# Optimization experiments

Measured on AMD Instinct MI355X. Metric: run time of the kernel, lower is better.

Reference implementation:

```python
import jax, jax.numpy as jnp
import numpy as np

N, B, PG, L, HC, EC, H, NC, KNN = 256, 4, 64, 32, 128, 64, 4, 14, 8
D = HC // H
CUTOFF = 10.0
LOG2 = 0.6931471805599453

_counts = np.array([14, 5, 11, 8, 8, 6, 9, 9, 4, 10, 8, 8, 9, 8, 11, 7, 6, 7, 14, 12, 7])
RES_ATOM_MASK = (np.arange(14)[None, :] < _counts[:, None]).astype(np.float32)  # [21,14]


def _ln(x, g, b):
    mu = jnp.mean(x, -1, keepdims=True)
    var = jnp.mean((x - mu) ** 2, -1, keepdims=True)
    return (x - mu) / jnp.sqrt(var + 1e-5) * g + b


def _ssp(x):
    return jax.nn.softplus(x) - LOG2


def _safe_norm(x):
    return jnp.sqrt(jnp.maximum(jnp.sum(x * x, -1), 1e-12))


def _seg_softmax(x, idx, n):
    m = jax.ops.segment_max(x, idx, num_segments=n)
    e = jnp.exp(x - m[idx])
    s = jax.ops.segment_sum(e, idx, num_segments=n)
    return e / s[idx]


def _smear(d):
    offs = jnp.linspace(0.0, CUTOFF, EC)
    coeff = -0.5 / (offs[1] - offs[0]) ** 2
    return jnp.exp(coeff * (d[..., None] - offs) ** 2)


def _core(res_H, res_X, ligand_pos, ligand_feat, ligand_mask,
          ln_g, ln_b, ln1_g, ln1_b,
          WQ, WK, WV, WKl, WVl, WO, WOl, WOl1,
          Ti_w1, Ti_b1, Ti_w2, Ti_b2,
          sD_w1, sD_b1, sD_w2, sD_b2,
          sD1_w1, sD1_b1, sD1_w2, sD1_b2,
          res_S, batch, residue_mask, row1, col1):
    n = res_H.shape[0]
    bsz = ligand_feat.shape[0]
    lc = ligand_feat.shape[1]
    amask = jnp.asarray(RES_ATOM_MASK)[res_S]  # [n,14]

    # kNN graph on C-alpha (atom 1), per-graph, flow target_to_source, + self loops
    ctr = res_X[:, 1]
    d2 = jnp.sum((ctr[:, None] - ctr[None]) ** 2, -1)
    bad = (batch[:, None] != batch[None]) | jnp.eye(n, dtype=bool)
    _, nbr = jax.lax.top_k(-jnp.where(bad, jnp.inf, d2), KNN)
    row = jnp.concatenate([jnp.repeat(jnp.arange(n), KNN), jnp.arange(n)])
    col = jnp.concatenate([nbr.reshape(-1), jnp.arange(n)])

    Rij = _safe_norm(res_X[row][:, :, None] - res_X[col][:, None])  # [E,14,14]
    drep = _smear(Rij)  # [E,14,14,EC]

    res_Hn = _ln(res_H, ln_g, ln_b)
    Q = (res_Hn @ WQ.T).reshape(n, NC, H, D)
    Kt = (res_Hn @ WK.T).reshape(n, NC, H, D)
    V = (res_Hn @ WV.T).reshape(n, NC, H, D)

    logits = jnp.einsum('ephd,eqhd->ehpq', Q[row], Kt[col]) / np.sqrt(D)
    sig = jax.nn.relu(drep @ sD_w1.T + sD_b1) @ sD_w2.T + sD_b2  # [E,14,14,H]
    logits = logits + sig.transpose(0, 3, 1, 2)

    am_e = amask[row][:, :, None] * amask[col][:, None]  # [E,14,14]
    r = jnp.einsum('ep,ehpq,eq->eh', amask[row], logits, amask[col])
    r = r / jnp.sum(am_e, (-1, -2))[:, None]
    beta = _seg_softmax(r, row, n)  # [E,H]

    att = jax.nn.softmax(logits, -1) * am_e[:, None]
    att = att / (jnp.sum(jnp.abs(att), -1, keepdims=True) + 1e-7)
    aV = jnp.einsum('ehpq,eqhd->ehpd', att, V[col])
    updH = jax.ops.segment_sum(beta[:, :, None, None] * aV, row, num_segments=n)
    updH = updH.transpose(0, 2, 1, 3).reshape(n, NC, HC)
    res_H2 = (res_Hn + _ssp(updH) @ WO.T) * amask[..., None]

    Xij = res_X[row][:, :, None] - res_X[col][:, None]  # [E,14,14,3]
    Xij = Xij / (_safe_norm(Xij)[..., None] + 1e-5)
    Qf = Q.reshape(n, NC, HC)
    Kf = Kt.reshape(n, NC, HC)
    # T_i on concat([Q_p, K_q, dist]) computed as split matmuls (no big concat)
    hmid = (Qf[row] @ Ti_w1[:, :HC].T)[:, :, None, :] \
        + (Kf[col] @ Ti_w1[:, HC:2 * HC].T)[:, None, :, :] \
        + drep @ Ti_w1[:, 2 * HC:].T + Ti_b1  # [E,14,14,HC]
    f = (jax.nn.relu(hmid) @ Ti_w2.T + Ti_b2)[..., 0]  # [E,14,14]
    f = f * jnp.mean(att, 1)
    dX = jax.ops.segment_sum(jnp.mean(beta, -1)[:, None, None]
                             * jnp.sum(f[..., None] * Xij, -2), row, num_segments=n)
    res_X2 = jnp.where(residue_mask[:, None, None],
                       res_X + jnp.clip(dX, -3.0, 3.0), res_X)

    # residue <-> ligand cross attention over (editable residue, graph) edges
    lf = _ln(ligand_feat, ln1_g, ln1_b)
    Kl = (lf @ WKl.T).reshape(bsz, lc, H, D)
    Vl = (lf @ WVl.T).reshape(bsz, lc, H, D)
    Rij1 = _safe_norm(res_X2[row1][:, :, None] - ligand_pos[col1][:, None])
    drep1 = _smear(Rij1)  # [E1,14,L,EC]
    lg = jnp.einsum('ephd,eqhd->ehpq', Q[row1], Kl[col1]) / np.sqrt(D)
    sig1 = jax.nn.relu(drep1 @ sD1_w1.T + sD1_b1) @ sD1_w2.T + sD1_b2
    lg = lg + sig1.transpose(0, 3, 1, 2)

    am1 = amask[row1][:, :, None] * ligand_mask[col1][:, None]  # [E1,14,L]
    r1 = jnp.einsum('ep,ehpq,eq->eh', amask[row1], lg, ligand_mask[col1])
    r1 = r1 / jnp.sum(am1, (-1, -2))[:, None]
    beta1 = _seg_softmax(r1, col1, bsz)

    ar = jax.nn.softmax(lg, -1) * am1[:, None]
    ar = ar / (jnp.sum(jnp.abs(ar), -1, keepdims=True) + 1e-7)
    al = jax.nn.softmax(lg, -2) * am1[:, None]
    # faithful to source: lig branch divided by L1 norm of already-normalized ar
    al = al / (jnp.sum(jnp.abs(ar), -1, keepdims=True) + 1e-7)
    aVr = jnp.einsum('ehpq,eqhd->ehpd', ar, Vl[col1])  # [E1,H,14,D]
    e1 = row1.shape[0]
    res_H3 = res_H2.at[row1].add(
        _ssp(aVr.transpose(0, 2, 1, 3).reshape(e1, NC, HC)) @ WOl.T)
    res_H3 = res_H3 * amask[..., None]
    aVlg = jnp.einsum('ehpq,ephd->ehqd', al, V[row1])  # [E1,H,L,D]
    updL = jax.ops.segment_sum(beta1[:, :, None, None] * aVlg, col1, num_segments=bsz)
    lf2 = lf + _ssp(updL.transpose(0, 2, 1, 3).reshape(bsz, lc, HC)) @ WOl1.T
    return res_H3, res_X2, lf2


def setup_inputs() -> dict:
    key = jax.random.key(0)
    ks = jax.random.split(key, 40)
    rn = lambda i, shape, s=1.0: jax.random.normal(ks[i], shape, jnp.float32) * s
    w = lambda i, shape: jax.random.normal(ks[i], shape, jnp.float32) * 0.05
    res_H = rn(0, (N, NC, HC))
    res_X = rn(1, (N, NC, 3), 4.0)
    res_S = jax.random.randint(ks[2], (N,), 0, 21)
    batch = jnp.repeat(jnp.arange(B), PG)
    residue_mask = (jnp.arange(N) % PG) < 16
    row1 = jnp.asarray(np.nonzero(np.asarray(residue_mask))[0])
    col1 = row1 // PG
    ligand_pos = rn(3, (B, L, 3), 4.0)
    ligand_feat = rn(4, (B, L, HC))
    ligand_mask = jnp.tile((jnp.arange(L) < 24).astype(jnp.float32)[None], (B, 1))
    return dict(
        res_H=res_H, res_X=res_X, ligand_pos=ligand_pos, ligand_feat=ligand_feat,
        ligand_mask=ligand_mask,
        ln_g=jnp.ones((HC,)), ln_b=jnp.zeros((HC,)),
        ln1_g=jnp.ones((HC,)), ln1_b=jnp.zeros((HC,)),
        WQ=w(5, (HC, HC)), WK=w(6, (HC, HC)), WV=w(7, (HC, HC)),
        WKl=w(8, (HC, HC)), WVl=w(9, (HC, HC)),
        WO=w(10, (HC, HC)), WOl=w(11, (HC, HC)), WOl1=w(12, (HC, HC)),
        Ti_w1=w(13, (HC, 2 * HC + EC)), Ti_b1=jnp.zeros((HC,)),
        Ti_w2=w(14, (1, HC)), Ti_b2=jnp.zeros((1,)),
        sD_w1=w(15, (HC, EC)), sD_b1=jnp.zeros((HC,)),
        sD_w2=w(16, (H, HC)), sD_b2=jnp.zeros((H,)),
        sD1_w1=w(17, (HC, EC)), sD1_b1=jnp.zeros((HC,)),
        sD1_w2=w(18, (H, HC)), sD1_b2=jnp.zeros((H,)),
        res_S=res_S, batch=batch, residue_mask=residue_mask, row1=row1, col1=col1)


def reference(res_H, res_X, ligand_pos, ligand_feat, ligand_mask,
              ln_g, ln_b, ln1_g, ln1_b,
              WQ, WK, WV, WKl, WVl, WO, WOl, WOl1,
              Ti_w1, Ti_b1, Ti_w2, Ti_b2,
              sD_w1, sD_b1, sD_w2, sD_b2,
              sD1_w1, sD1_b1, sD1_w2, sD1_b2,
              res_S, batch, residue_mask, row1, col1):
    return _core(res_H, res_X, ligand_pos, ligand_feat, ligand_mask,
                 ln_g, ln_b, ln1_g, ln1_b,
                 WQ, WK, WV, WKl, WVl, WO, WOl, WOl1,
                 Ti_w1, Ti_b1, Ti_w2, Ti_b2,
                 sD_w1, sD_b1, sD_w2, sD_b2,
                 sD1_w1, sD1_b1, sD1_w2, sD1_b2,
                 res_S, batch, residue_mask, row1, col1)
```

## Files before the change

kernel.cpp:

```cpp
#include <hip/hip_runtime.h>
#include <hip/hip_bf16.h>
#include <math.h>

typedef __hip_bfloat16 bf16;

#define NRES 256
#define LC   32
#define HCH  128
#define ECH  64
#define NH   4
#define NCA  14
#define KNNK 8
#define DH   32
#define NKE  (NRES*KNNK)
#define NEDGE (NKE+NRES)
#define NE1  64
#define NROWS (NRES*NCA)

#define NT     3073
#define TSCALE 256.0f
#define DMAXT  12.0f

#define O_RESH   0
#define O_RESX   458752
#define O_LPOS   469504
#define O_LFEAT  469888
#define O_LMASK  486272
#define O_LNG    486400
#define O_LNB    486528
#define O_LN1G   486656
#define O_LN1B   486784
#define O_WQ     486912
#define O_WK     503296
#define O_WV     519680
#define O_WKL    536064
#define O_WVL    552448
#define O_WO     568832
#define O_WOL    585216
#define O_WOL1   601600
#define O_TIW1   617984
#define O_TIB1   658944
#define O_TIW2   659072
#define O_TIB2   659200
#define O_SDW1   659204
#define O_SDB1   667396
#define O_SDW2   667524
#define O_SDB2   668036
#define O_SD1W1  668040
#define O_SD1B1  676232
#define O_SD1W2  676360
#define O_SD1B2  676872
#define TOTCVT   676876
#define CVT_RSV  676880

#define OUTX_OFF 458752
#define OUTL_OFF 469504

#define NGEMM 291
#define FCV   476
#define FG0   (FCV+1)
#define FTR0  (FG0+NGEMM)
#define FTOT  (FTR0+640)

__constant__ int c_counts[21] = {14,5,11,8,8,6,9,9,4,10,8,8,9,8,11,7,6,7,14,12,7};

using bfrag = __attribute__((ext_vector_type(8))) short;
using f32x4 = __attribute__((ext_vector_type(4))) float;

__device__ __forceinline__ float b2f(bf16 x){ return __bfloat162float(x); }
__device__ __forceinline__ float sspf(float x){
  return fmaxf(x,0.f) + log1pf(expf(-fabsf(x))) - 0.6931471805599453f;
}
__device__ __forceinline__ float bflo(unsigned u){ return __uint_as_float(u<<16); }
__device__ __forceinline__ float bfhi(unsigned u){ return __uint_as_float(u & 0xffff0000u); }
__device__ __forceinline__ unsigned short f2bs(float v){ bf16 b=__float2bfloat16(v); return *(unsigned short*)&b; }
__device__ __forceinline__ unsigned pack2(float a, float b){
  return (unsigned)f2bs(a) | ((unsigned)f2bs(b)<<16);
}
__device__ __forceinline__ int ccount(int s){ return c_counts[s<0?0:(s>20?20:s)]; }
__device__ __forceinline__ void storeOut(void* out, int isbf, int idx, float v){
  if (isbf) ((bf16*)out)[idx] = __float2bfloat16(v);
  else      ((float*)out)[idx] = v;
}
__device__ __forceinline__ float rdv(const void* p, int isbf, int i){
  return isbf ? b2f(((const bf16*)p)[i]) : ((const float*)p)[i];
}

__global__ __launch_bounds__(256) void kfront(
    const void* s0,const void* s1,const void* s2,const void* s3,const void* s4,
    const void* s5,const void* s6,const void* s7,const void* s8,const void* s9,
    const void* s10,const void* s11,const void* s12,const void* s13,const void* s14,
    const void* s15,const void* s16,const void* s17,const void* s18,const void* s19,
    const void* s20,const void* s21,const void* s22,const void* s23,const void* s24,
    const void* s25,const void* s26,const void* s27,const void* s28,
    const int* __restrict__ row1,
    float* __restrict__ dst, int* __restrict__ flag,
    unsigned* __restrict__ ctab, float* __restrict__ sig1T,
    float* __restrict__ wt, int* __restrict__ inv_row)
{
  int bb = blockIdx.x, tid = threadIdx.x;
  __shared__ int sflag;
  if (tid < 64){
    unsigned w = ((const unsigned*)s0)[tid];
    unsigned lo = w & 0xFFFFu;
    int ee = (lo >> 7) & 0xFF;
    int good = (lo == 0u) || (ee >= 121 && ee <= 133);
    unsigned long long m = __ballot(good);
    if (tid == 0){
      sflag = (__popcll(m) >= 40) ? 1 : 0;
      if (bb == 0) flag[0] = sflag;
    }
  }
  __syncthreads();
  int isbf = sflag;

  if (bb < FCV){
    int g0 = (bb*256 + tid)*4;
    if (g0 >= O_WQ) return;
    const void* src; int l;
    if      (g0 < O_RESX ) { src=s0; l=g0; }
    else if (g0 < O_LPOS ) { src=s1; l=g0-O_RESX; }
    else if (g0 < O_LFEAT) { src=s2; l=g0-O_LPOS; }
    else if (g0 < O_LMASK) { src=s3; l=g0-O_LFEAT; }
    else if (g0 < O_LNG  ) { src=s4; l=g0-O_LMASK; }
    else if (g0 < O_LNB  ) { src=s5; l=g0-O_LNG; }
    else if (g0 < O_LN1G ) { src=s6; l=g0-O_LNB; }
    else if (g0 < O_LN1B ) { src=s7; l=g0-O_LN1G; }
    else                   { src=s8; l=g0-O_LN1B; }
    float4 o4;
    if (isbf){
      uint2 u = *(const uint2*)((const unsigned short*)src + l);
      o4.x = bflo(u.x); o4.y = bfhi(u.x); o4.z = bflo(u.y); o4.w = bfhi(u.y);
    } else {
      o4 = *(const float4*)((const float*)src + l);
    }
    *(float4*)(dst + g0) = o4;
    return;
  }

  if (bb == FCV){
    if (tid < 132){
      int g = O_TIW2 + tid;
      float v = (g < O_TIB2) ? rdv(s19, isbf, g - O_TIW2) : rdv(s20, isbf, 0);
      dst[g] = v;
    }
    inv_row[tid] = -1;
    __syncthreads();
    if (tid < NE1) inv_row[row1[tid] & 255] = tid;
    return;
  }

  if (bb < FTR0){
    __shared__ float Wl[128*68];
    __shared__ float Et[32*68];
    __shared__ float H[32*132];
    __shared__ float W2[4*132];
    __shared__ float W2b[4];
    int gb = bb - FG0;
    int mt = gb % 97, m = gb / 97;
    int r0 = mt*32;
    int nr = (NT - r0 < 32) ? (NT - r0) : 32;

    for (int idx=tid; idx<8192; idx+=256){
      int o=idx>>6, k=idx&63;
      float v = (m==0) ? rdv(s17, isbf, o*320 + 256 + k)
              : (m==1) ? rdv(s21, isbf, idx)
                       : rdv(s25, isbf, idx);
      Wl[o*68+k] = v;
    }
    {
      const float step = 10.0f/63.0f;
      const float coef = -0.5f/(step*step);
      for (int idx=tid; idx<2048; idx+=256){
        int r=idx>>6, k=idx&63;
        float t = (float)(r0+r)*(1.0f/256.0f) - step*(float)k;
        Et[r*68+k] = expf(coef*t*t);
      }
    }
    if (m >= 1){
      const void* w2p = (m==1)? s23 : s27;
      const void* b2p = (m==1)? s24 : s28;
      for (int idx=tid; idx<512; idx+=256)
        W2[(idx>>7)*132 + (idx&127)] = rdv(w2p, isbf, idx);
      if (tid < 4) W2b[tid] = rdv(b2p, isbf, tid);
    }
    __syncthreads();

    int o = tid & 127, g = tid >> 7;
    const void* bp = (m==0)? s18 : (m==1)? s22 : s26;
    float bias = rdv(bp, isbf, o);
    float acc[16];
    #pragma unroll
    for (int i=0;i<16;i++) acc[i] = bias;
    const float* wrow = Wl + o*68;
    const float* ebase = Et + g*16*68;
    for (int kc=0; kc<16; kc++){
      float4 w4 = *(const float4*)(wrow + kc*4);
      #pragma unroll
      for (int i=0;i<16;i++){
        float4 e4 = *(const float4*)(ebase + i*68 + kc*4);
        acc[i] += e4.x*w4.x;
        acc[i] += e4.y*w4.y;
        acc[i] += e4.z*w4.z;
        acc[i] += e4.w*w4.w;
      }
    }

    if (m == 0){
      #pragma unroll
      for (int i=0;i<16;i++){
        int row = r0 + g*16 + i;
        float c = acc[i];
// ... 25 lines not shown
          float s1 = __shfl_down(s,1);
          float s2 = __shfl_down(s,2);
          float s3 = __shfl_down(s,3);
          if (hh == 0){
            ctab[(size_t)row*68 + 0] = pack2(s, s1);
            ctab[(size_t)row*68 + 1] = pack2(s2, s3);
          }
        } else {
          sig1T[row*4 + hh] = s;
        }
      }
    }
    return;
  }

  {
    int gid = (bb - FTR0)*256 + tid;
    int m = gid >> 14;
    int j = gid & 16383;
    int oo = j >> 7, c = j & 127;
    float v;
    switch(m){
      case 0: v = rdv(s9,  isbf, j); break;
      case 1: v = rdv(s10, isbf, j); break;
      case 2: v = rdv(s11, isbf, j); break;
      case 3: v = rdv(s14, isbf, j); break;
      case 4: v = rdv(s12, isbf, j); break;
      case 5: v = rdv(s13, isbf, j); break;
      case 6: v = rdv(s15, isbf, j); break;
      case 7: v = rdv(s16, isbf, j); break;
      case 8: v = rdv(s17, isbf, oo*320 + c); break;
      default:v = rdv(s17, isbf, oo*320 + 128 + c); break;
    }
    wt[m*16384 + c*128 + oo] = v;
  }
}

__global__ __launch_bounds__(256) void kProjAll(
    const float* __restrict__ cvt, const float* __restrict__ wt, const int* __restrict__ batch,
    float* __restrict__ resHn, bf16* __restrict__ Qw16, bf16* __restrict__ Kw16,
    bf16* __restrict__ Vw16, bf16* __restrict__ TQw16, bf16* __restrict__ TKw16,
    int* __restrict__ nbr, float* __restrict__ lf, bf16* __restrict__ Klw16, bf16* __restrict__ Vlw16)
{
  __shared__ float Xs[16*129];
  __shared__ float x2[2][HCH];
  __shared__ float sred2[2][2];
  int bb = blockIdx.x, tid = threadIdx.x;

  if (bb < 672){
    int m = bb / 224;
    int rt = (bb % 224) * 16;
    for (int i=tid; i<16*128; i+=256){
      int r=i>>7, c=i&127;
      Xs[r*129+c] = cvt[O_RESH + (rt+r)*HCH + c];
    }
    __syncthreads();
    {
      int wave = tid>>6, lane = tid&63;
      int r = wave*4 + (lane>>4);
      int cb = lane & 15;
      float s=0;
      #pragma unroll
      for (int j=0;j<8;j++) s += Xs[r*129 + cb + 16*j];
      #pragma unroll
      for (int off=1; off<16; off<<=1) s += __shfl_xor(s, off);
      float mu = s*(1.f/HCH);
      float q=0;
      #pragma unroll
      for (int j=0;j<8;j++){ float dv = Xs[r*129+cb+16*j]-mu; q += dv*dv; }
      #pragma unroll
      for (int off=1; off<16; off<<=1) q += __shfl_xor(q, off);
      float inv = rsqrtf(q*(1.f/HCH) + 1e-5f);
      #pragma unroll
      for (int j=0;j<8;j++){
        int c = cb + 16*j;
        float xh = (Xs[r*129+c]-mu)*inv*cvt[O_LNG+c] + cvt[O_LNB+c];
        Xs[r*129+c] = xh;
        if (m==0) resHn[(rt+r)*HCH+c] = xh;
      }
    }
    __syncthreads();
    int tc = (tid & 31) * 4;
    int tr = (tid >> 5) * 2;
    const float* W = wt + m*16384;
    float a00=0,a01=0,a02=0,a03=0, a10=0,a11=0,a12=0,a13=0;
    for (int c=0;c<HCH;c++){
      float4 w4 = *(const float4*)(W + c*128 + tc);
      float x0 = Xs[tr*129 + c];
      float x1 = Xs[(tr+1)*129 + c];
      a00 += x0*w4.x; a01 += x0*w4.y; a02 += x0*w4.z; a03 += x0*w4.w;
      a10 += x1*w4.x; a11 += x1*w4.y; a12 += x1*w4.z; a13 += x1*w4.w;
    }
    bf16* out = (m==0)? Qw16 : (m==1)? Kw16 : Vw16;
    {
      unsigned* o0 = (unsigned*)(out + (rt+tr  )*HCH + tc);
      unsigned* o1 = (unsigned*)(out + (rt+tr+1)*HCH + tc);
      o0[0]=pack2(a00,a01); o0[1]=pack2(a02,a03);
      o1[0]=pack2(a10,a11); o1[1]=pack2(a12,a13);
    }
    if (m == 2) return;
    __syncthreads();
    Xs[tr*129+tc]=a00; Xs[tr*129+tc+1]=a01; Xs[tr*129+tc+2]=a02; Xs[tr*129+tc+3]=a03;
    Xs[(tr+1)*129+tc]=a10; Xs[(tr+1)*129+tc+1]=a11; Xs[(tr+1)*129+tc+2]=a12; Xs[(tr+1)*129+tc+3]=a13;
    __syncthreads();
    const float* W2 = wt + (8+m)*16384;
    a00=0;a01=0;a02=0;a03=0; a10=0;a11=0;a12=0;a13=0;
    for (int c=0;c<HCH;c++){
      float4 w4 = *(const float4*)(W2 + c*128 + tc);
      float x0 = Xs[tr*129 + c];
      float x1 = Xs[(tr+1)*129 + c];
      a00 += x0*w4.x; a01 += x0*w4.y; a02 += x0*w4.z; a03 += x0*w4.w;
      a10 += x1*w4.x; a11 += x1*w4.y; a12 += x1*w4.z; a13 += x1*w4.w;
    }
    bf16* out2 = m ? TKw16 : TQw16;
    {
      unsigned* o0 = (unsigned*)(out2 + (rt+tr  )*HCH + tc);
      unsigned* o1 = (unsigned*)(out2 + (rt+tr+1)*HCH + tc);
      o0[0]=pack2(a00,a01); o0[1]=pack2(a02,a03);
      o1[0]=pack2(a10,a11); o1[1]=pack2(a12,a13);
    }
    return;
  }

  if (bb < 736){
    int wave = tid>>6, lane = tid&63;
    int n = (bb-672)*4 + wave;
    float cx = cvt[O_RESX+(n*NCA+1)*3+0];
    float cy = cvt[O_RESX+(n*NCA+1)*3+1];
    float cz = cvt[O_RESX+(n*NCA+1)*3+2];
    int bn = batch[n];
    float d2v[4]; int idv[4];
    #pragma unroll
    for (int t=0;t<4;t++){
      int j = lane + 64*t;
      float jx = cvt[O_RESX+(j*NCA+1)*3+0];
      float jy = cvt[O_RESX+(j*NCA+1)*3+1];
      float jz = cvt[O_RESX+(j*NCA+1)*3+2];
      float dx=cx-jx, dy=cy-jy, dz=cz-jz;
      float d2 = dx*dx+dy*dy+dz*dz;
      bool bad = (batch[j]!=bn) || (j==n);
      d2v[t] = bad ? INFINITY : d2;
      idv[t] = j;
    }
    for (int k=0;k<KNNK;k++){
      float dm = d2v[0]; int im = idv[0];
      #pragma unroll
      for (int t=1;t<4;t++)
        if (d2v[t]<dm || (d2v[t]==dm && idv[t]<im)){ dm=d2v[t]; im=idv[t]; }
      #pragma unroll
      for (int off=1; off<64; off<<=1){
        float dn = __shfl_xor(dm, off);
        int   in = __shfl_xor(im, off);
        if (dn<dm || (dn==dm && in<im)){ dm=dn; im=in; }
      }
      if (lane==0) nbr[n*KNNK+k] = im;
      #pragma unroll
      for (int t=0;t<4;t++) if (idv[t]==im) d2v[t] = INFINITY;
    }
    return;
  }

  int row = tid>>7, t = tid&127;
  int rb = (bb-736)*2 + row;
  float v = cvt[O_LFEAT + rb*HCH + t];
  float s=v;
  for (int off=1; off<64; off<<=1) s += __shfl_xor(s, off);
  if ((t&63)==0) sred2[row][t>>6]=s;
  __syncthreads();
  float mu=(sred2[row][0]+sred2[row][1])*(1.f/HCH);
  __syncthreads();
  float d=v-mu; s=d*d;
  for (int off=1; off<64; off<<=1) s += __shfl_xor(s, off);
  if ((t&63)==0) sred2[row][t>>6]=s;
  __syncthreads();
  float var=(sred2[row][0]+sred2[row][1])*(1.f/HCH);
  float xh = d*rsqrtf(var+1e-5f)*cvt[O_LN1G+t] + cvt[O_LN1B+t];
  x2[row][t]=xh; lf[rb*HCH+t]=xh;
  __syncthreads();
  const float* WKlt = wt + 4*16384;
  const float* WVlt = wt + 5*16384;
  float aK=0.f, aV=0.f;
  for (int c=0;c<HCH;c++){
    float xc=x2[row][c];
    aK += xc*WKlt[c*128+t];
    aV += xc*WVlt[c*128+t];
  }
  Klw16[rb*HCH+t]=__float2bfloat16(aK);
  Vlw16[rb*HCH+t]=__float2bfloat16(aV);
}

#define PR1(cbu, tau, kau, wl, wh) \
  fa += fmaxf(bflo(tau)+bflo(kau)+bflo(cbu),0.f)*(wl) + fmaxf(bfhi(tau)+bfhi(kau)+bfhi(cbu),0.f)*(wh);

__global__ __launch_bounds__(256) void k3_edge(
    const float* __restrict__ cvt, const int* __restrict__ res_S, const int* __restrict__ nbr,
    const bf16* __restrict__ Qw16, const bf16* __restrict__ Kw16,
    const bf16* __restrict__ TQw16, const bf16* __restrict__ TKw16,
    const bf16* __restrict__ Vw16, const unsigned* __restrict__ ctab,
    float* __restrict__ r_ws, bf16* __restrict__ aVe16, float* __restrict__ dXe)
{
  __shared__ __align__(16) unsigned char UB[8192];
  __shared__ unsigned Tqp[14*66], Tkp[14*66];
  __shared__ float LG[4*16*17];
// ... 195 lines not shown
    #pragma unroll
    for (int qq=0;qq<NCA;qq++){
      float diff = Xr[pp*3+jx]-Xc[qq*3+jx];
      a += FR[pp*14+qq]*diff;
    }
    dXe[(e*NCA+pp)*3+jx] = a;
  }
}

__global__ __launch_bounds__(256) void k4_agg(
    const float* __restrict__ cvt, const int* __restrict__ res_S, const int* __restrict__ inv_row,
    const float* __restrict__ r_ws, const bf16* __restrict__ aVe16, const float* __restrict__ dXe,
    const float* __restrict__ resHn, const float* __restrict__ wt, const int* __restrict__ flag,
    float* __restrict__ resH2, float* __restrict__ resX2, void* __restrict__ d_out)
{
  int n = blockIdx.x, tid = threadIdx.x;
  __shared__ float beta[9][NH];
  __shared__ float betam[9];
  __shared__ float Xs[NCA][HCH];
  if (tid < NH){
    int h = tid;
    float rv[9], m=-INFINITY;
    #pragma unroll
    for (int k=0;k<9;k++){
      int ek = (k<KNNK)? n*KNNK+k : NKE+n;
      rv[k] = r_ws[ek*NH+h];
      m = fmaxf(m, rv[k]);
    }
    float s=0;
    #pragma unroll
    for (int k=0;k<9;k++){ rv[k]=expf(rv[k]-m); s+=rv[k]; }
    #pragma unroll
    for (int k=0;k<9;k++) beta[k][h]=rv[k]/s;
  }
  __syncthreads();
  if (tid < 9) betam[tid] = 0.25f*(beta[tid][0]+beta[tid][1]+beta[tid][2]+beta[tid][3]);
  int col = tid & 127, ph = tid >> 7;
  int h = col>>5, dd = col&31;
  float bh[9];
  #pragma unroll
  for (int k=0;k<9;k++) bh[k]=beta[k][h];
  #pragma unroll
  for (int i=0;i<7;i++){
    int p = ph + 2*i;
    float u=0;
    #pragma unroll
    for (int k=0;k<9;k++){
      int ek = (k<KNNK)? n*KNNK+k : NKE+n;
      u += bh[k]*b2f(aVe16[ek*1792 + h*448 + p*32 + dd]);
    }
    Xs[p][col] = sspf(u);
  }
  __syncthreads();
  const float* WOt = wt + 3*16384;
  float acc[7];
  #pragma unroll
  for (int i=0;i<7;i++) acc[i]=0.f;
  for (int c=0;c<HCH;c++){
    float w = WOt[c*128+col];
    #pragma unroll
    for (int i=0;i<7;i++) acc[i] += Xs[ph+2*i][c]*w;
  }
  int cnt = ccount(res_S[n]);
  #pragma unroll
  for (int i=0;i<7;i++){
    int p = ph + 2*i;
    float am = (p<cnt)?1.f:0.f;
    float outv = (resHn[(n*NCA+p)*HCH+col] + acc[i])*am;
    resH2[(n*NCA+p)*HCH+col] = outv;
  }
  if (tid < NCA*3){
    int isbf = *flag;
    int p=tid/3, jx=tid%3;
    float s=0;
    #pragma unroll
    for (int k=0;k<9;k++){
      int ek=(k<KNNK)? n*KNNK+k : NKE+n;
      s += betam[k]*dXe[(ek*NCA+p)*3+jx];
    }
    float base = cvt[O_RESX+(n*NCA+p)*3+jx];
    float v = (inv_row[n]>=0) ? base + fminf(fmaxf(s,-3.f),3.f) : base;
    resX2[(n*NCA+p)*3+jx] = v;
    storeOut(d_out, isbf, OUTX_OFF + (n*NCA+p)*3+jx, v);
  }
}

// ... 37 lines not shown

  const float isq=0.17677669529663687f;
  for (int pair=tid; pair<448; pair+=256){
    int p=pair>>5, q=pair&31;
    float dx=Xr[p*3]-Lp[q*3], dy=Xr[p*3+1]-Lp[q*3+1], dz=Xr[p*3+2]-Lp[q*3+2];
    float d=sqrtf(fmaxf(dx*dx+dy*dy+dz*dz,1e-12f));
    int i0=(int)(fminf(d,DMAXT)*TSCALE+0.5f);
    float sg = sig1T[i0*4+h];
    float qk=0;
    #pragma unroll
    for (int dd=0;dd<DH;dd++) qk += Bq[p*33+dd]*Bk[q*33+dd];
    LG[p*33+q] = qk*isq + sg;
  }
  __syncthreads();

  if (tid < 14){
    int pp=tid; float ap=amr[pp];
    float s=0, m=-INFINITY;
    for (int qq=0;qq<LC;qq++){ float v=LG[pp*33+qq]; s+=v*lm[qq]; m=fmaxf(m,v); }
    rpart[pp]=s*ap;
    float sum=0;
    for (int qq=0;qq<LC;qq++) sum+=expf(LG[pp*33+qq]-m);
    float inv=1.f/sum, s2=0;
    for (int qq=0;qq<LC;qq++) s2+=expf(LG[pp*33+qq]-m)*inv*ap*lm[qq];
    s2r[pp]=s2/(s2+1e-7f);
  }
  if (tid==14){ float sr=0; for(int i=0;i<14;i++) sr+=amr[i]; cnts[0]=sr; }
  if (tid==15){ float sl=0; for(int i=0;i<32;i++) sl+=lm[i]; cnts[1]=sl; }
  __syncthreads();

  if (tid==0){ float s=0; for (int pp=0;pp<14;pp++) s+=rpart[pp]; r1_ws[e*NH+h]=s/(cnts[0]*cnts[1]); }
  if (tid < 32){
    int qq=tid;
    float m=-INFINITY;
    for (int pp=0;pp<14;pp++) m=fmaxf(m,LG[pp*33+qq]);
    float sum=0;
    for (int pp=0;pp<14;pp++) sum+=expf(LG[pp*33+qq]-m);
    float inv=1.f/sum, lq=lm[qq];
    for (int pp=0;pp<14;pp++){
      float a=expf(LG[pp*33+qq]-m)*inv*amr[pp]*lq;
      ALs[pp*33+qq]=a/(s2r[pp]+1e-7f);
    }
  }
  __syncthreads();

  if (tid < 14){
    int pp=tid; float ap=amr[pp];
    float m=-INFINITY;
    for (int qq=0;qq<LC;qq++) m=fmaxf(m,LG[pp*33+qq]);
    float row[LC]; float sum=0;
    for (int qq=0;qq<LC;qq++){ row[qq]=expf(LG[pp*33+qq]-m); sum+=row[qq]; }
    float inv=1.f/sum, s2=0;
    for (int qq=0;qq<LC;qq++){ row[qq]=row[qq]*inv*ap*lm[qq]; s2+=row[qq]; }
    float inv2=1.f/(s2+1e-7f);
    for (int qq=0;qq<LC;qq++) LG[pp*33+qq]=row[qq]*inv2;
  }
  __syncthreads();

  for (int j=tid;j<448;j+=256){
    int pp=j>>5, dd=j&31;
    float acc=0;
    #pragma unroll
    for (int qq=0;qq<LC;qq++) acc += LG[pp*33+qq]*Vls[qq*33+dd];
    aVr[e*1792 + h*448 + j]=acc;
  }
  for (int j=tid;j<1024;j+=256){
    int qq=j>>5, dd=j&31;
    float acc=0;
    #pragma unroll
    for (int pp=0;pp<14;pp++) acc += ALs[pp*33+qq]*Vrs[pp*33+dd];
    aVlg[e*4096 + h*1024 + j]=acc;
  }
}

__global__ __launch_bounds__(256) void k78_final(
    const int* __restrict__ inv_row, const int* __restrict__ res_S, const int* __restrict__ col1,
    const float* __restrict__ resH2, const float* __restrict__ aVr,
    const float* __restrict__ r1_ws, const float* __restrict__ aVlg, const float* __restrict__ lf,
    const float* __restrict__ wt, const int* __restrict__ flag, void* __restrict__ d_out)
{
  int bb = blockIdx.x, tid = threadIdx.x;
  if (bb < 256){
    int n = bb;
    int e = inv_row[n];
    __shared__ float G[NCA][HCH];
// ... 16 lines not shown
        for (int i=0;i<7;i++) acc[i]+=G[ph+2*i][c]*w;
      }
    }
    int cnt=ccount(res_S[n]);
    int isbf = *flag;
    #pragma unroll
    for (int i=0;i<7;i++){
      int p = ph + 2*i;
      float am=(p<cnt)?1.f:0.f;
      float v=(resH2[(n*NCA+p)*HCH+col]+acc[i])*am;
      storeOut(d_out, isbf, (n*NCA+p)*HCH+col, v);
    }
    return;
  }
  int rb = bb - 256;
  int b = rb>>5, q = rb&31;
  __shared__ float bw[NE1][NH];
  __shared__ float xs[HCH];
  if (tid<NH){
    int h=tid;
    float m=-INFINITY;
    for (int e=0;e<NE1;e++) if ((col1[e]&3)==b) m=fmaxf(m, r1_ws[e*NH+h]);
    float s=0;
    for (int e=0;e<NE1;e++) if ((col1[e]&3)==b) s+=expf(r1_ws[e*NH+h]-m);
    for (int e=0;e<NE1;e++) bw[e][h] = ((col1[e]&3)==b)? expf(r1_ws[e*NH+h]-m)/s : 0.f;
  }
  __syncthreads();
  if (tid < 128){
    int h=tid>>5, dd=tid&31;
    float u=0;
    for (int e=0;e<NE1;e++) u += bw[e][h]*aVlg[e*4096 + h*1024 + q*32 + dd];
    xs[tid]=sspf(u);
  }
  __syncthreads();
  if (tid < 128){
    const float* WOl1t = wt + 7*16384;
    float acc=0;
    for (int c=0;c<HCH;c++) acc += xs[c]*WOl1t[c*128+tid];
    float v = lf[rb*HCH+tid] + acc;
    storeOut(d_out, *flag, OUTL_OFF + rb*HCH+tid, v);
// ... 24 lines not shown
  bf16*  TKw16   = (bf16*)(wsf + o); o += NROWS*HCH/2;
  float* r_ws    = wsf + o; o += NEDGE*NH;
  bf16*  aVe16   = (bf16*)(wsf + o); o += (size_t)NEDGE*1792/2;
  float* dXe     = wsf + o; o += NEDGE*NCA*3;
  float* resH2   = wsf + o; o += NROWS*HCH;
  float* resX2   = wsf + o; o += NRES*NCA*3;
  float* lf      = wsf + o; o += 4*LC*HCH;
  bf16*  Klw16   = (bf16*)(wsf + o); o += 4*LC*HCH/2;
  bf16*  Vlw16   = (bf16*)(wsf + o); o += 4*LC*HCH/2;
  float* r1w     = wsf + o; o += NE1*NH;
  float* aVrw    = wsf + o; o += NE1*1792;
  float* aVlgw   = wsf + o; o += NE1*4096;
  unsigned* ctab = (unsigned*)(wsf + o); o += (size_t)NT*68;
  float* sig1T   = wsf + o; o += NT*4;

  kfront<<<FTOT, 256, 0, stream>>>(
      d_in[0],d_in[1],d_in[2],d_in[3],d_in[4],d_in[5],d_in[6],d_in[7],d_in[8],
      d_in[9],d_in[10],d_in[11],d_in[12],d_in[13],d_in[14],d_in[15],d_in[16],
      d_in[17],d_in[18],d_in[19],d_in[20],d_in[21],d_in[22],d_in[23],d_in[24],
      d_in[25],d_in[26],d_in[27],d_in[28],
      row1, cvt, flag, ctab, sig1T, wt, inv_row);
  kProjAll<<<800, 256, 0, stream>>>(cvt, wt, batch, resHn, Qw16, Kw16, Vw16, TQw16, TKw16,
                                    nbr, lf, Klw16, Vlw16);
  k3_edge<<<NEDGE, 256, 0, stream>>>(cvt, res_S, nbr, Qw16, Kw16, TQw16, TKw16, Vw16, ctab,
                                     r_ws, aVe16, dXe);
  k4_agg<<<NRES, 256, 0, stream>>>(cvt, res_S, inv_row, r_ws, aVe16, dXe, resHn, wt, flag,
                                   resH2, resX2, d_out);
  k6_lig<<<NE1*NH, 256, 0, stream>>>(cvt, res_S, row1, col1, resX2, Qw16, Klw16, Vw16, Vlw16, sig1T,
                                     r1w, aVrw, aVlgw);
  k78_final<<<384, 256, 0, stream>>>(inv_row, res_S, col1, resH2, aVrw, r1w, aVlgw, lf,
                                     wt, flag, d_out);
}
```

Measured before the change: 239.0 us.

## Merge projection kernel into front kernel and parallelize aggregation and softmax stages

Fuses the former kProjAll work (LayerNorm and Q/K/V/TQ/TK projections, kNN, ligand projections) into the front conversion kernel, reading raw inputs directly instead of the converted and transposed copies. This removes one kernel launch and the dependency on the conversion pass, at the cost of reading weights in their original layout from global memory. The edge-table GEMM also stops staging weights in shared memory. Separately, k4_agg is split over two blocks per residue, the k6_lig row softmax is spread across 224 threads with shuffle reductions instead of 14 serial threads, and the k78 ligand softmax weights are computed by all threads in parallel.

```diff
diff --git a/kernel.cpp b/kernel.cpp
--- a/kernel.cpp
+++ b/kernel.cpp
@@ -31,25 +31,8 @@
 #define O_LN1G   486656
 #define O_LN1B   486784
 #define O_WQ     486912
-#define O_WK     503296
-#define O_WV     519680
-#define O_WKL    536064
-#define O_WVL    552448
-#define O_WO     568832
-#define O_WOL    585216
-#define O_WOL1   601600
-#define O_TIW1   617984
-#define O_TIB1   658944
 #define O_TIW2   659072
 #define O_TIB2   659200
-#define O_SDW1   659204
-#define O_SDB1   667396
-#define O_SDW2   667524
-#define O_SDB2   668036
-#define O_SD1W1  668040
-#define O_SD1B1  676232
-#define O_SD1W2  676360
-#define O_SD1B2  676872
 #define TOTCVT   676876
 #define CVT_RSV  676880
 
@@ -60,7 +43,10 @@
 #define FCV   476
 #define FG0   (FCV+1)
 #define FTR0  (FG0+NGEMM)
-#define FTOT  (FTR0+640)
+#define FPJ0  (FTR0+640)
+#define FKN0  (FPJ0+672)
+#define FLG0  (FKN0+64)
+#define FBTOT (FLG0+64)
 
 __constant__ int c_counts[21] = {14,5,11,8,8,6,9,9,4,10,8,8,9,8,11,7,6,7,14,12,7};
 
@@ -85,21 +71,36 @@
 __device__ __forceinline__ float rdv(const void* p, int isbf, int i){
   return isbf ? b2f(((const bf16*)p)[i]) : ((const float*)p)[i];
 }
-
-__global__ __launch_bounds__(256) void kfront(
+__device__ __forceinline__ float4 rd4(const void* p, int isbf, int i){
+  float4 r;
+  if (isbf){
+    uint2 u = *(const uint2*)((const unsigned short*)p + i);
+    r.x=bflo(u.x); r.y=bfhi(u.x); r.z=bflo(u.y); r.w=bfhi(u.y);
+  } else {
+    r = *(const float4*)((const float*)p + i);
+  }
+  return r;
+}
+
+__global__ __launch_bounds__(256) void kbig(
     const void* s0,const void* s1,const void* s2,const void* s3,const void* s4,
     const void* s5,const void* s6,const void* s7,const void* s8,const void* s9,
     const void* s10,const void* s11,const void* s12,const void* s13,const void* s14,
     const void* s15,const void* s16,const void* s17,const void* s18,const void* s19,
     const void* s20,const void* s21,const void* s22,const void* s23,const void* s24,
     const void* s25,const void* s26,const void* s27,const void* s28,
-    const int* __restrict__ row1,
+    const int* __restrict__ row1, const int* __restrict__ batch,
     float* __restrict__ dst, int* __restrict__ flag,
     unsigned* __restrict__ ctab, float* __restrict__ sig1T,
-    float* __restrict__ wt, int* __restrict__ inv_row)
+    float* __restrict__ wt, int* __restrict__ inv_row,
+    float* __restrict__ resHn, bf16* __restrict__ Qw16, bf16* __restrict__ Kw16,
+    bf16* __restrict__ Vw16, bf16* __restrict__ TQw16, bf16* __restrict__ TKw16,
+    int* __restrict__ nbr, float* __restrict__ lf,
+    bf16* __restrict__ Klw16, bf16* __restrict__ Vlw16)
 {
+  __shared__ __align__(16) unsigned char SH[27760];
+  __shared__ int sflag;
   int bb = blockIdx.x, tid = threadIdx.x;
-  __shared__ int sflag;
   if (tid < 64){
     unsigned w = ((const unsigned*)s0)[tid];
     unsigned lo = w & 0xFFFFu;
@@ -127,13 +128,7 @@
     else if (g0 < O_LN1G ) { src=s6; l=g0-O_LNB; }
     else if (g0 < O_LN1B ) { src=s7; l=g0-O_LN1G; }
     else                   { src=s8; l=g0-O_LN1B; }
-    float4 o4;
-    if (isbf){
-      uint2 u = *(const uint2*)((const unsigned short*)src + l);
-      o4.x = bflo(u.x); o4.y = bfhi(u.x); o4.z = bflo(u.y); o4.w = bfhi(u.y);
-    } else {
-      o4 = *(const float4*)((const float*)src + l);
-    }
+    float4 o4 = rd4(src, isbf, l);
     *(float4*)(dst + g0) = o4;
     return;
   }
@@ -151,23 +146,14 @@
   }
 
   if (bb < FTR0){
-    __shared__ float Wl[128*68];
-    __shared__ float Et[32*68];
-    __shared__ float H[32*132];
-    __shared__ float W2[4*132];
-    __shared__ float W2b[4];
+    float* Et  = (float*)SH;
+    float* H   = (float*)(SH + 8704);
+    float* W2  = (float*)(SH + 25600);
+    float* W2b = (float*)(SH + 27712);
     int gb = bb - FG0;
     int mt = gb % 97, m = gb / 97;
     int r0 = mt*32;
     int nr = (NT - r0 < 32) ? (NT - r0) : 32;
-
-    for (int idx=tid; idx<8192; idx+=256){
-      int o=idx>>6, k=idx&63;
-      float v = (m==0) ? rdv(s17, isbf, o*320 + 256 + k)
-              : (m==1) ? rdv(s21, isbf, idx)
-                       : rdv(s25, isbf, idx);
-      Wl[o*68+k] = v;
-    }
     {
       const float step = 10.0f/63.0f;
       const float coef = -0.5f/(step*step);
@@ -187,15 +173,17 @@
     __syncthreads();
 
     int o = tid & 127, g = tid >> 7;
-    const void* bp = (m==0)? s18 : (m==1)? s22 : s26;
+    const void* bp  = (m==0)? s18 : (m==1)? s22 : s26;
+    const void* sWp = (m==0)? s17 : (m==1)? s21 : s25;
+    int wstride = (m==0)? 320 : 64;
+    int wadd    = (m==0)? 256 : 0;
     float bias = rdv(bp, isbf, o);
     float acc[16];
     #pragma unroll
     for (int i=0;i<16;i++) acc[i] = bias;
-    const float* wrow = Wl + o*68;
     const float* ebase = Et + g*16*68;
     for (int kc=0; kc<16; kc++){
-      float4 w4 = *(const float4*)(wrow + kc*4);
+      float4 w4 = rd4(sWp, isbf, o*wstride + wadd + kc*4);
       #pragma unroll
       for (int i=0;i<16;i++){
         float4 e4 = *(const float4*)(ebase + i*68 + kc*4);
@@ -251,7 +239,7 @@
     return;
   }
 
-  {
+  if (bb < FPJ0){
     int gid = (bb - FTR0)*256 + tid;
     int m = gid >> 14;
     int j = gid & 16383;
@@ -270,26 +258,21 @@
       default:v = rdv(s17, isbf, oo*320 + 128 + c); break;
     }
     wt[m*16384 + c*128 + oo] = v;
-  }
-}
-
-__global__ __launch_bounds__(256) void kProjAll(
-    const float* __restrict__ cvt, const float* __restrict__ wt, const int* __restrict__ batch,
-    float* __restrict__ resHn, bf16* __restrict__ Qw16, bf16* __restrict__ Kw16,
-    bf16* __restrict__ Vw16, bf16* __restrict__ TQw16, bf16* __restrict__ TKw16,
-    int* __restrict__ nbr, float* __restrict__ lf, bf16* __restrict__ Klw16, bf16* __restrict__ Vlw16)
-{
-  __shared__ float Xs[16*129];
-  __shared__ float x2[2][HCH];
-  __shared__ float sred2[2][2];
-  int bb = blockIdx.x, tid = threadIdx.x;
-
-  if (bb < 672){
-    int m = bb / 224;
-    int rt = (bb % 224) * 16;
-    for (int i=tid; i<16*128; i+=256){
-      int r=i>>7, c=i&127;
-      Xs[r*129+c] = cvt[O_RESH + (rt+r)*HCH + c];
+    return;
+  }
+
+  if (bb < FKN0){
+    float* Xs = (float*)SH;
+    int idx = bb - FPJ0;
+    int m = idx / 224;
+    int rt = (idx % 224) * 16;
+    const void* sW = (m==0)? s9 : (m==1)? s10 : s11;
+    #pragma unroll
+    for (int k=0;k<2;k++){
+      int v = tid + k*256;
+      int r = v>>5, c4 = (v&31)*4;
+      float4 x = rd4(s0, isbf, (rt+r)*HCH + c4);
+      *(float4*)(Xs + r*132 + c4) = x;
     }
     __syncthreads();
     {
@@ -298,35 +281,43 @@
       int cb = lane & 15;
       float s=0;
       #pragma unroll
-      for (int j=0;j<8;j++) s += Xs[r*129 + cb + 16*j];
+      for (int j=0;j<8;j++) s += Xs[r*132 + cb + 16*j];
       #pragma unroll
       for (int off=1; off<16; off<<=1) s += __shfl_xor(s, off);
       float mu = s*(1.f/HCH);
       float q=0;
       #pragma unroll
-      for (int j=0;j<8;j++){ float dv = Xs[r*129+cb+16*j]-mu; q += dv*dv; }
+      for (int j=0;j<8;j++){ float dv = Xs[r*132+cb+16*j]-mu; q += dv*dv; }
       #pragma unroll
       for (int off=1; off<16; off<<=1) q += __shfl_xor(q, off);
       float inv = rsqrtf(q*(1.f/HCH) + 1e-5f);
       #pragma unroll
       for (int j=0;j<8;j++){
         int c = cb + 16*j;
-        float xh = (Xs[r*129+c]-mu)*inv*cvt[O_LNG+c] + cvt[O_LNB+c];
-        Xs[r*129+c] = xh;
+        float xh = (Xs[r*132+c]-mu)*inv*rdv(s5,isbf,c) + rdv(s6,isbf,c);
+        Xs[r*132+c] = xh;
         if (m==0) resHn[(rt+r)*HCH+c] = xh;
       }
     }
     __syncthreads();
     int tc = (tid & 31) * 4;
     int tr = (tid >> 5) * 2;
-    const float* W = wt + m*16384;
     float a00=0,a01=0,a02=0,a03=0, a10=0,a11=0,a12=0,a13=0;
-    for (int c=0;c<HCH;c++){
-      float4 w4 = *(const float4*)(W + c*128 + tc);
-      float x0 = Xs[tr*129 + c];
-      float x1 = Xs[(tr+1)*129 + c];
-      a00 += x0*w4.x; a01 += x0*w4.y; a02 += x0*w4.z; a03 += x0*w4.w;
-      a10 += x1*w4.x; a11 += x1*w4.y; a12 += x1*w4.z; a13 += x1*w4.w;
+    for (int c=0;c<HCH;c+=4){
+      float4 w0 = rd4(sW, isbf, (tc+0)*HCH + c);
+      float4 w1 = rd4(sW, isbf, (tc+1)*HCH + c);
+      float4 w2 = rd4(sW, isbf, (tc+2)*HCH + c);
+      float4 w3 = rd4(sW, isbf, (tc+3)*HCH + c);
+      float4 x0 = *(const float4*)(Xs + tr*132 + c);
+      float4 x1 = *(const float4*)(Xs + (tr+1)*132 + c);
+      a00 += x0.x*w0.x; a00 += x0.y*w0.y; a00 += x0.z*w0.z; a00 += x0.w*w0.w;
+      a01 += x0.x*w1.x; a01 += x0.y*w1.y; a01 += x0.z*w1.z; a01 += x0.w*w1.w;
+      a02 += x0.x*w2.x; a02 += x0.y*w2.y; a02 += x0.z*w2.z; a02 += x0.w*w2.w;
+      a03 += x0.x*w3.x; a03 += x0.y*w3.y; a03 += x0.z*w3.z; a03 += x0.w*w3.w;
+      a10 += x1.x*w0.x; a10 += x1.y*w0.y; a10 += x1.z*w0.z; a10 += x1.w*w0.w;
+      a11 += x1.x*w1.x; a11 += x1.y*w1.y; a11 += x1.z*w1.z; a11 += x1.w*w1.w;
+      a12 += x1.x*w2.x; a12 += x1.y*w2.y; a12 += x1.z*w2.z; a12 += x1.w*w2.w;
+      a13 += x1.x*w3.x; a13 += x1.y*w3.y; a13 += x1.z*w3.z; a13 += x1.w*w3.w;
     }
     bf16* out = (m==0)? Qw16 : (m==1)? Kw16 : Vw16;
     {
@@ -337,17 +328,26 @@
     }
     if (m == 2) return;
     __syncthreads();
-    Xs[tr*129+tc]=a00; Xs[tr*129+tc+1]=a01; Xs[tr*129+tc+2]=a02; Xs[tr*129+tc+3]=a03;
-    Xs[(tr+1)*129+tc]=a10; Xs[(tr+1)*129+tc+1]=a11; Xs[(tr+1)*129+tc+2]=a12; Xs[(tr+1)*129+tc+3]=a13;
-    __syncthreads();
-    const float* W2 = wt + (8+m)*16384;
+    Xs[tr*132+tc]=a00; Xs[tr*132+tc+1]=a01; Xs[tr*132+tc+2]=a02; Xs[tr*132+tc+3]=a03;
+    Xs[(tr+1)*132+tc]=a10; Xs[(tr+1)*132+tc+1]=a11; Xs[(tr+1)*132+tc+2]=a12; Xs[(tr+1)*132+tc+3]=a13;
+    __syncthreads();
+    int moff = m*128;
     a00=0;a01=0;a02=0;a03=0; a10=0;a11=0;a12=0;a13=0;
-    for (int c=0;c<HCH;c++){
-      float4 w4 = *(const float4*)(W2 + c*128 + tc);
-      float x0 = Xs[tr*129 + c];
-      float x1 = Xs[(tr+1)*129 + c];
-      a00 += x0*w4.x; a01 += x0*w4.y; a02 += x0*w4.z; a03 += x0*w4.w;
-      a10 += x1*w4.x; a11 += x1*w4.y; a12 += x1*w4.z; a13 += x1*w4.w;
+    for (int c=0;c<HCH;c+=4){
+      float4 w0 = rd4(s17, isbf, (tc+0)*320 + moff + c);
+      float4 w1 = rd4(s17, isbf, (tc+1)*320 + moff + c);
+      float4 w2 = rd4(s17, isbf, (tc+2)*320 + moff + c);
+      float4 w3 = rd4(s17, isbf, (tc+3)*320 + moff + c);
+      float4 x0 = *(const float4*)(Xs + tr*132 + c);
+      float4 x1 = *(const float4*)(Xs + (tr+1)*132 + c);
+      a00 += x0.x*w0.x; a00 += x0.y*w0.y; a00 += x0.z*w0.z; a00 += x0.w*w0.w;
+      a01 += x0.x*w1.x; a01 += x0.y*w1.y; a01 += x0.z*w1.z; a01 += x0.w*w1.w;
+      a02 += x0.x*w2.x; a02 += x0.y*w2.y; a02 += x0.z*w2.z; a02 += x0.w*w2.w;
+      a03 += x0.x*w3.x; a03 += x0.y*w3.y; a03 += x0.z*w3.z; a03 += x0.w*w3.w;
+      a10 += x1.x*w0.x; a10 += x1.y*w0.y; a10 += x1.z*w0.z; a10 += x1.w*w0.w;
+      a11 += x1.x*w1.x; a11 += x1.y*w1.y; a11 += x1.z*w1.z; a11 += x1.w*w1.w;
+      a12 += x1.x*w2.x; a12 += x1.y*w2.y; a12 += x1.z*w2.z; a12 += x1.w*w2.w;
+      a13 += x1.x*w3.x; a13 += x1.y*w3.y; a13 += x1.z*w3.z; a13 += x1.w*w3.w;
     }
     bf16* out2 = m ? TKw16 : TQw16;
     {
@@ -359,20 +359,20 @@
     return;
   }
 
-  if (bb < 736){
+  if (bb < FLG0){
     int wave = tid>>6, lane = tid&63;
-    int n = (bb-672)*4 + wave;
-    float cx = cvt[O_RESX+(n*NCA+1)*3+0];
-    float cy = cvt[O_RESX+(n*NCA+1)*3+1];
-    float cz = cvt[O_RESX+(n*NCA+1)*3+2];
+    int n = (bb-FKN0)*4 + wave;
+    float cx = rdv(s1, isbf, (n*NCA+1)*3+0);
+    float cy = rdv(s1, isbf, (n*NCA+1)*3+1);
+    float cz = rdv(s1, isbf, (n*NCA+1)*3+2);
     int bn = batch[n];
     float d2v[4]; int idv[4];
     #pragma unroll
     for (int t=0;t<4;t++){
       int j = lane + 64*t;
-      float jx = cvt[O_RESX+(j*NCA+1)*3+0];
-      float jy = cvt[O_RESX+(j*NCA+1)*3+1];
-      float jz = cvt[O_RESX+(j*NCA+1)*3+2];
+      float jx = rdv(s1, isbf, (j*NCA+1)*3+0);
+      float jy = rdv(s1, isbf, (j*NCA+1)*3+1);
+      float jz = rdv(s1, isbf, (j*NCA+1)*3+2);
       float dx=cx-jx, dy=cy-jy, dz=cz-jz;
       float d2 = dx*dx+dy*dy+dz*dz;
       bool bad = (batch[j]!=bn) || (j==n);
@@ -397,33 +397,37 @@
     return;
   }
 
-  int row = tid>>7, t = tid&127;
-  int rb = (bb-736)*2 + row;
-  float v = cvt[O_LFEAT + rb*HCH + t];
-  float s=v;
-  for (int off=1; off<64; off<<=1) s += __shfl_xor(s, off);
-  if ((t&63)==0) sred2[row][t>>6]=s;
-  __syncthreads();
-  float mu=(sred2[row][0]+sred2[row][1])*(1.f/HCH);
-  __syncthreads();
-  float d=v-mu; s=d*d;
-  for (int off=1; off<64; off<<=1) s += __shfl_xor(s, off);
-  if ((t&63)==0) sred2[row][t>>6]=s;
-  __syncthreads();
-  float var=(sred2[row][0]+sred2[row][1])*(1.f/HCH);
-  float xh = d*rsqrtf(var+1e-5f)*cvt[O_LN1G+t] + cvt[O_LN1B+t];
-  x2[row][t]=xh; lf[rb*HCH+t]=xh;
-  __syncthreads();
-  const float* WKlt = wt + 4*16384;
-  const float* WVlt = wt + 5*16384;
-  float aK=0.f, aV=0.f;
-  for (int c=0;c<HCH;c++){
-    float xc=x2[row][c];
-    aK += xc*WKlt[c*128+t];
-    aV += xc*WVlt[c*128+t];
-  }
-  Klw16[rb*HCH+t]=__float2bfloat16(aK);
-  Vlw16[rb*HCH+t]=__float2bfloat16(aV);
+  {
+    float* x2    = (float*)SH;
+    float* sred2 = (float*)(SH + 1024);
+    int row = tid>>7, t = tid&127;
+    int rb = (bb-FLG0)*2 + row;
+    float v = rdv(s3, isbf, rb*HCH + t);
+    float s=v;
+    for (int off=1; off<64; off<<=1) s += __shfl_xor(s, off);
+    if ((t&63)==0) sred2[row*2 + (t>>6)]=s;
+    __syncthreads();
+    float mu=(sred2[row*2]+sred2[row*2+1])*(1.f/HCH);
+    __syncthreads();
+    float d=v-mu; s=d*d;
+    for (int off=1; off<64; off<<=1) s += __shfl_xor(s, off);
+    if ((t&63)==0) sred2[row*2 + (t>>6)]=s;
+    __syncthreads();
+    float var=(sred2[row*2]+sred2[row*2+1])*(1.f/HCH);
+    float xh = d*rsqrtf(var+1e-5f)*rdv(s7,isbf,t) + rdv(s8,isbf,t);
+    x2[row*128+t]=xh; lf[rb*HCH+t]=xh;
+    __syncthreads();
+    float aK=0.f, aV=0.f;
+    for (int c=0;c<HCH;c+=4){
+      float4 x  = *(const float4*)(x2 + row*128 + c);
+      float4 wk = rd4(s12, isbf, t*HCH + c);
+      float4 wv = rd4(s13, isbf, t*HCH + c);
+      aK += x.x*wk.x; aK += x.y*wk.y; aK += x.z*wk.z; aK += x.w*wk.w;
+      aV += x.x*wv.x; aV += x.y*wv.y; aV += x.z*wv.z; aV += x.w*wv.w;
+    }
+    Klw16[rb*HCH+t]=__float2bfloat16(aK);
+    Vlw16[rb*HCH+t]=__float2bfloat16(aV);
+  }
 }
 
 #define PR1(cbu, tau, kau, wl, wh) \
@@ -649,10 +653,11 @@
     const float* __restrict__ resHn, const float* __restrict__ wt, const int* __restrict__ flag,
     float* __restrict__ resH2, float* __restrict__ resX2, void* __restrict__ d_out)
 {
-  int n = blockIdx.x, tid = threadIdx.x;
+  int b = blockIdx.x, tid = threadIdx.x;
+  int n = b >> 1, half = b & 1;
   __shared__ float beta[9][NH];
   __shared__ float betam[9];
-  __shared__ float Xs[NCA][HCH];
+  __shared__ float Xs[7][HCH];
   if (tid < NH){
     int h = tid;
     float rv[9], m=-INFINITY;
@@ -670,41 +675,46 @@
   }
   __syncthreads();
   if (tid < 9) betam[tid] = 0.25f*(beta[tid][0]+beta[tid][1]+beta[tid][2]+beta[tid][3]);
-  int col = tid & 127, ph = tid >> 7;
+  int col = tid & 127, sub = tid >> 7;
   int h = col>>5, dd = col&31;
+  int j0 = sub*4;
+  int jn = sub ? 3 : 4;
   float bh[9];
   #pragma unroll
   for (int k=0;k<9;k++) bh[k]=beta[k][h];
   #pragma unroll
-  for (int i=0;i<7;i++){
-    int p = ph + 2*i;
-    float u=0;
-    #pragma unroll
-    for (int k=0;k<9;k++){
-      int ek = (k<KNNK)? n*KNNK+k : NKE+n;
-      u += bh[k]*b2f(aVe16[ek*1792 + h*448 + p*32 + dd]);
-    }
-    Xs[p][col] = sspf(u);
+  for (int jj=0;jj<4;jj++){
+    if (jj < jn){
+      int p = half + 2*(j0+jj);
+      float u=0;
+      #pragma unroll
+      for (int k=0;k<9;k++){
+        int ek = (k<KNNK)? n*KNNK+k : NKE+n;
+        u += bh[k]*b2f(aVe16[(size_t)ek*1792 + h*448 + p*32 + dd]);
+      }
+      Xs[j0+jj][col] = sspf(u);
+    }
   }
   __syncthreads();
   const float* WOt = wt + 3*16384;
-  float acc[7];
-  #pragma unroll
-  for (int i=0;i<7;i++) acc[i]=0.f;
+  float acc[4] = {0.f,0.f,0.f,0.f};
   for (int c=0;c<HCH;c++){
     float w = WOt[c*128+col];
     #pragma unroll
-    for (int i=0;i<7;i++) acc[i] += Xs[ph+2*i][c]*w;
+    for (int jj=0;jj<4;jj++)
+      if (jj < jn) acc[jj] += Xs[j0+jj][c]*w;
   }
   int cnt = ccount(res_S[n]);
   #pragma unroll
-  for (int i=0;i<7;i++){
-    int p = ph + 2*i;
-    float am = (p<cnt)?1.f:0.f;
-    float outv = (resHn[(n*NCA+p)*HCH+col] + acc[i])*am;
-    resH2[(n*NCA+p)*HCH+col] = outv;
-  }
-  if (tid < NCA*3){
+  for (int jj=0;jj<4;jj++){
+    if (jj < jn){
+      int p = half + 2*(j0+jj);
+      float am = (p<cnt)?1.f:0.f;
+      float outv = (resHn[(n*NCA+p)*HCH+col] + acc[jj])*am;
+      resH2[(n*NCA+p)*HCH+col] = outv;
+    }
+  }
+  if (half==0 && tid < NCA*3){
     int isbf = *flag;
     int p=tid/3, jx=tid%3;
     float s=0;
@@ -772,46 +782,56 @@
   }
   __syncthreads();
 
-  if (tid < 14){
-    int pp=tid; float ap=amr[pp];
-    float s=0, m=-INFINITY;
-    for (int qq=0;qq<LC;qq++){ float v=LG[pp*33+qq]; s+=v*lm[qq]; m=fmaxf(m,v); }
-    rpart[pp]=s*ap;
-    float sum=0;
-    for (int qq=0;qq<LC;qq++) sum+=expf(LG[pp*33+qq]-m);
-    float inv=1.f/sum, s2=0;
-    for (int qq=0;qq<LC;qq++) s2+=expf(LG[pp*33+qq]-m)*inv*ap*lm[qq];
-    s2r[pp]=s2/(s2+1e-7f);
-  }
-  if (tid==14){ float sr=0; for(int i=0;i<14;i++) sr+=amr[i]; cnts[0]=sr; }
-  if (tid==15){ float sl=0; for(int i=0;i<32;i++) sl+=lm[i]; cnts[1]=sl; }
-  __syncthreads();
-
-  if (tid==0){ float s=0; for (int pp=0;pp<14;pp++) s+=rpart[pp]; r1_ws[e*NH+h]=s/(cnts[0]*cnts[1]); }
+  float a0=0.f, a1=0.f;
+  if (tid < 224){
+    int pp = tid>>4, qh = tid&15;
+    float v0 = LG[pp*33+qh], v1 = LG[pp*33+qh+16];
+    float l0 = lm[qh], l1 = lm[qh+16];
+    float sl = v0*l0 + v1*l1;
+    float mx = fmaxf(v0,v1);
+    #pragma unroll
+    for (int off=1; off<16; off<<=1){
+      sl += __shfl_xor(sl,off);
+      mx = fmaxf(mx, __shfl_xor(mx,off));
+    }
+    float e0=expf(v0-mx), e1=expf(v1-mx);
+    float se=e0+e1;
+    #pragma unroll
+    for (int off=1; off<16; off<<=1) se += __shfl_xor(se,off);
+    float inv=1.f/se, ap=amr[pp];
+    float t0=e0*inv*ap*l0, t1=e1*inv*ap*l1;
+    float s2=t0+t1;
+    #pragma unroll
+    for (int off=1; off<16; off<<=1) s2 += __shfl_xor(s2,off);
+    float inv2=1.f/(s2+1e-7f);
+    a0=t0*inv2; a1=t1*inv2;
+    if (qh==0){ rpart[pp]=sl*ap; s2r[pp]=s2*inv2; }
+  } else if (tid == 224){
+    float sr=0; for (int i=0;i<NCA;i++) sr+=amr[i]; cnts[0]=sr;
+  } else if (tid == 225){
+    float sl=0; for (int i=0;i<LC;i++) sl+=lm[i]; cnts[1]=sl;
+  }
+  __syncthreads();
+
+  if (tid==0){ float s=0; for (int pp=0;pp<NCA;pp++) s+=rpart[pp]; r1_ws[e*NH+h]=s/(cnts[0]*cnts[1]); }
   if (tid < 32){
     int qq=tid;
     float m=-INFINITY;
-    for (int pp=0;pp<14;pp++) m=fmaxf(m,LG[pp*33+qq]);
+    for (int pp=0;pp<NCA;pp++) m=fmaxf(m,LG[pp*33+qq]);
     float sum=0;
-    for (int pp=0;pp<14;pp++) sum+=expf(LG[pp*33+qq]-m);
+    for (int pp=0;pp<NCA;pp++) sum+=expf(LG[pp*33+qq]-m);
     float inv=1.f/sum, lq=lm[qq];
-    for (int pp=0;pp<14;pp++){
+    for (int pp=0;pp<NCA;pp++){
       float a=expf(LG[pp*33+qq]-m)*inv*amr[pp]*lq;
       ALs[pp*33+qq]=a/(s2r[pp]+1e-7f);
     }
   }
   __syncthreads();
 
-  if (tid < 14){
-    int pp=tid; float ap=amr[pp];
-    float m=-INFINITY;
-    for (int qq=0;qq<LC;qq++) m=fmaxf(m,LG[pp*33+qq]);
-    float row[LC]; float sum=0;
-    for (int qq=0;qq<LC;qq++){ row[qq]=expf(LG[pp*33+qq]-m); sum+=row[qq]; }
-    float inv=1.f/sum, s2=0;
-    for (int qq=0;qq<LC;qq++){ row[qq]=row[qq]*inv*ap*lm[qq]; s2+=row[qq]; }
-    float inv2=1.f/(s2+1e-7f);
-    for (int qq=0;qq<LC;qq++) LG[pp*33+qq]=row[qq]*inv2;
+  if (tid < 224){
+    int pp = tid>>4, qh = tid&15;
+    LG[pp*33+qh]    = a0;
+    LG[pp*33+qh+16] = a1;
   }
   __syncthreads();
 
@@ -826,7 +846,7 @@
     int qq=j>>5, dd=j&31;
     float acc=0;
     #pragma unroll
-    for (int pp=0;pp<14;pp++) acc += ALs[pp*33+qq]*Vrs[pp*33+dd];
+    for (int pp=0;pp<NCA;pp++) acc += ALs[pp*33+qq]*Vrs[pp*33+dd];
     aVlg[e*4096 + h*1024 + j]=acc;
   }
 }
@@ -873,16 +893,25 @@
     return;
   }
   int rb = bb - 256;
-  int b = rb>>5, q = rb&31;
+  int bsel = rb>>5, q = rb&31;
   __shared__ float bw[NE1][NH];
   __shared__ float xs[HCH];
-  if (tid<NH){
-    int h=tid;
-    float m=-INFINITY;
-    for (int e=0;e<NE1;e++) if ((col1[e]&3)==b) m=fmaxf(m, r1_ws[e*NH+h]);
-    float s=0;
-    for (int e=0;e<NE1;e++) if ((col1[e]&3)==b) s+=expf(r1_ws[e*NH+h]-m);
-    for (int e=0;e<NE1;e++) bw[e][h] = ((col1[e]&3)==b)? expf(r1_ws[e*NH+h]-m)/s : 0.f;
+  __shared__ float r1s[256];
+  __shared__ int cls[64];
+  r1s[tid] = r1_ws[tid];
+  if (tid < 64) cls[tid] = col1[tid] & 3;
+  __syncthreads();
+  {
+    int e = tid>>2, h = tid&3;
+    float v = 0.f;
+    if (cls[e] == bsel){
+      float m = -INFINITY;
+      for (int ee=0; ee<NE1; ee++) if (cls[ee]==bsel) m = fmaxf(m, r1s[ee*4+h]);
+      float s = 0;
+      for (int ee=0; ee<NE1; ee++) if (cls[ee]==bsel) s += expf(r1s[ee*4+h]-m);
+      v = expf(r1s[tid]-m)/s;
+    }
+    bw[e][h] = v;
   }
   __syncthreads();
   if (tid < 128){
@@ -937,18 +966,17 @@
   unsigned* ctab = (unsigned*)(wsf + o); o += (size_t)NT*68;
   float* sig1T   = wsf + o; o += NT*4;
 
-  kfront<<<FTOT, 256, 0, stream>>>(
+  kbig<<<FBTOT, 256, 0, stream>>>(
       d_in[0],d_in[1],d_in[2],d_in[3],d_in[4],d_in[5],d_in[6],d_in[7],d_in[8],
       d_in[9],d_in[10],d_in[11],d_in[12],d_in[13],d_in[14],d_in[15],d_in[16],
       d_in[17],d_in[18],d_in[19],d_in[20],d_in[21],d_in[22],d_in[23],d_in[24],
       d_in[25],d_in[26],d_in[27],d_in[28],
-      row1, cvt, flag, ctab, sig1T, wt, inv_row);
-  kProjAll<<<800, 256, 0, stream>>>(cvt, wt, batch, resHn, Qw16, Kw16, Vw16, TQw16, TKw16,
-                                    nbr, lf, Klw16, Vlw16);
+      row1, batch, cvt, flag, ctab, sig1T, wt, inv_row,
+      resHn, Qw16, Kw16, Vw16, TQw16, TKw16, nbr, lf, Klw16, Vlw16);
   k3_edge<<<NEDGE, 256, 0, stream>>>(cvt, res_S, nbr, Qw16, Kw16, TQw16, TKw16, Vw16, ctab,
                                      r_ws, aVe16, dXe);
-  k4_agg<<<NRES, 256, 0, stream>>>(cvt, res_S, inv_row, r_ws, aVe16, dXe, resHn, wt, flag,
-                                   resH2, resX2, d_out);
+  k4_agg<<<2*NRES, 256, 0, stream>>>(cvt, res_S, inv_row, r_ws, aVe16, dXe, resHn, wt, flag,
+                                     resH2, resX2, d_out);
   k6_lig<<<NE1*NH, 256, 0, stream>>>(cvt, res_S, row1, col1, resX2, Qw16, Klw16, Vw16, Vlw16, sig1T,
                                      r1w, aVrw, aVlgw);
   k78_final<<<384, 256, 0, stream>>>(inv_row, res_S, col1, resH2, aVrw, r1w, aVlgw, lf,
```

New measurement: 357.1 us. 49.4% more time.
